# Performance work log

Measured on AMD Instinct MI355X. Metric: run time of the kernel, lower is better.

Reference implementation:

```python
import jax, jax.numpy as jnp
import numpy as np

# Module hyperparameters (init_kwargs)
THRESHOLD_ABS = 0.2
THRESHOLD_REL = 0.05   # set to None to disable the relative-threshold branch
MIN_DISTANCE = 3


def setup_inputs() -> dict:
    key = jax.random.key(0)
    # belief maps in [0, 1), NCHW
    belive_map = jax.random.uniform(key, (32, 4, 512, 512), dtype=jnp.float32)
    return {"belive_map": belive_map}


def reference(belive_map):
    """Peak detection on belief maps (dense, jit-friendly form).

    Faithful to BeliveMapsNMS.forward: the torch module additionally compacts
    the mask into (coords, labels, scores) lists via nonzero/gather, which has
    data-dependent shapes; here we return the equivalent dense outputs:
      mask        [B,C,H,W] bool   - peak locations (nonzero of this == torch ind)
      scores_abs  [B,C,H,W] f32    - belief value at peaks, 0 elsewhere
      scores_rel  [B,C,H,W] f32    - scores_abs / per-(b,c) max
    """
    k = 2 * MIN_DISTANCE + 1          # 7
    pad = k // 2                       # 3 -> 'same' max pool, stride 1

    # F.max_pool2d(kernel=k, stride=1, padding=k//2)
    x_max = jax.lax.reduce_window(
        belive_map, -jnp.inf, jax.lax.max,
        window_dimensions=(1, 1, k, k),
        window_strides=(1, 1, 1, 1),
        padding=[(0, 0), (0, 0), (pad, pad), (pad, pad)],
    )

    # per-(batch, channel) global max: hh.max(dim=2) on the flattened map
    vmax = jnp.max(belive_map, axis=(2, 3), keepdims=True)  # [B,C,1,1]

    mask = (x_max == belive_map) & (belive_map > THRESHOLD_ABS)
    if THRESHOLD_REL is not None:
        mask = mask & (belive_map > THRESHOLD_REL * vmax)

    scores_abs = jnp.where(mask, belive_map, jnp.float32(0.0))
    scores_rel = scores_abs / vmax
    return mask, scores_abs, scores_rel
```

## Files before the change

### kernel.cpp

```cpp
#include <hip/hip_runtime.h>
#include <math.h>


#define H 512
#define W 512
#define PLANE_ELEMS (H * W)
#define TH 16
#define NROWS 14
#define RW 520
#define NEG_INF (-INFINITY)
#define VCHUNKS 16

typedef float v4f __attribute__((ext_vector_type(4)));

__device__ __forceinline__ float4 vmax4(float4 a, float4 b) {
    return make_float4(fmaxf(a.x, b.x), fmaxf(a.y, b.y), fmaxf(a.z, b.z), fmaxf(a.w, b.w));
}

__device__ __forceinline__ void nt_store4(float* p, float a, float b, float c, float d) {
    v4f v = {a, b, c, d};
    __builtin_nontemporal_store(v, (v4f*)p);
}

__global__ __launch_bounds__(256) void vmax_kernel(const float* __restrict__ in,
                                                   float* __restrict__ partials) {
    const int chunk = blockIdx.x;
    const int plane = blockIdx.y;
    const float4* p = (const float4*)(in + (size_t)plane * PLANE_ELEMS) + chunk * 4096;
    float4 v[16];
    #pragma unroll
    for (int j = 0; j < 16; ++j) v[j] = p[threadIdx.x + (j << 8)];
    float4 t[8];
    #pragma unroll
    for (int j = 0; j < 8; ++j) t[j] = vmax4(v[j], v[j + 8]);
    #pragma unroll
    for (int j = 0; j < 4; ++j) t[j] = vmax4(t[j], t[j + 4]);
    float4 q = vmax4(vmax4(t[0], t[1]), vmax4(t[2], t[3]));
    float m = fmaxf(fmaxf(q.x, q.y), fmaxf(q.z, q.w));
    #pragma unroll
    for (int o = 32; o > 0; o >>= 1) m = fmaxf(m, __shfl_down(m, o, 64));
    __shared__ float s[4];
    if ((threadIdx.x & 63) == 0) s[threadIdx.x >> 6] = m;
    __syncthreads();
    if (threadIdx.x == 0) {
        partials[(plane << 4) + chunk] = fmaxf(fmaxf(s[0], s[1]), fmaxf(s[2], s[3]));
    }
}

__global__ __launch_bounds__(256, 4) void nms_kernel(const float* __restrict__ in,
                                                     const float* __restrict__ partials,
                                                     float* __restrict__ out, int N) {
    const int hwid = blockIdx.x + (blockIdx.y << 5);
    const int wg = ((hwid & 7) << 9) + (hwid >> 3);
    const int plane = wg >> 5;
    const int ty0 = (wg & 31) * TH;

    const float* pin = in + (size_t)plane * PLANE_ELEMS;

    __shared__ __align__(16) float sCol[TH * RW];

    const int cg = threadIdx.x & 127;
    const int strip = threadIdx.x >> 7;
    const int c = cg << 2;
    const int y0 = strip << 3;
    const int gy0 = ty0 + y0;

    float4 r[NROWS];
    #pragma unroll
    for (int k = 0; k < NROWS; ++k) {
        const int gy = gy0 + k - 3;
        if (gy >= 0 && gy < H) {
            r[k] = *(const float4*)(pin + (size_t)gy * W + c);
        } else {
            r[k] = make_float4(NEG_INF, NEG_INF, NEG_INF, NEG_INF);
        }
    }

    float4 A[7];
    A[6] = r[6];
    #pragma unroll
    for (int j = 5; j >= 0; --j) A[j] = vmax4(r[j], A[j + 1]);
    float4 cm[8];
    cm[0] = A[0];
    float4 Bv = r[7];
    cm[1] = vmax4(A[1], Bv);
    #pragma unroll
    for (int j = 2; j <= 6; ++j) { Bv = vmax4(Bv, r[j + 6]); cm[j] = vmax4(A[j], Bv); }
    Bv = vmax4(Bv, r[13]);
    cm[7] = Bv;

    #pragma unroll
    for (int i = 0; i < 8; ++i) {
        *(float4*)&sCol[(y0 + i) * RW + 4 + c] = cm[i];
    }
    if (threadIdx.x < TH) {
        *(float4*)&sCol[threadIdx.x * RW] =
            make_float4(NEG_INF, NEG_INF, NEG_INF, NEG_INF);
    } else if (threadIdx.x < 2 * TH) {
        *(float4*)&sCol[(threadIdx.x - TH) * RW + 4 + W] =
            make_float4(NEG_INF, NEG_INF, NEG_INF, NEG_INF);
    }

    float4 pm0 = *(const float4*)&partials[(plane << 4) + 0];
    float4 pm1 = *(const float4*)&partials[(plane << 4) + 4];
    float4 pm2 = *(const float4*)&partials[(plane << 4) + 8];
    float4 pm3 = *(const float4*)&partials[(plane << 4) + 12];
    float4 q = vmax4(vmax4(pm0, pm1), vmax4(pm2, pm3));
    const float vmax = fmaxf(fmaxf(q.x, q.y), fmaxf(q.z, q.w));
    const float rel_thr = 0.05f * vmax;
    const float inv_vmax = 1.0f / vmax;

    __syncthreads();

    float* __restrict__ omask = out;
    float* __restrict__ oabs = out + (size_t)N;
    float* __restrict__ orel = out + 2 * (size_t)N;

    #pragma unroll
    for (int i = 0; i < 8; ++i) {
        const int rowb = (y0 + i) * RW;
        const float4 lo = *(const float4*)&sCol[rowb + c];
        const float4 hi = *(const float4*)&sCol[rowb + c + 8];
        const float a0 = lo.y, a1 = lo.z, a2 = lo.w;
        const float a3 = cm[i].x, a4 = cm[i].y, a5 = cm[i].z, a6 = cm[i].w;
        const float a7 = hi.x, a8 = hi.y, a9 = hi.z;
        const float t5 = fmaxf(a5, a6), t4 = fmaxf(a4, t5), t3 = fmaxf(a3, t4);
        const float t2 = fmaxf(a2, t3), t1 = fmaxf(a1, t2), t0 = fmaxf(a0, t1);
        const float b2 = fmaxf(a7, a8), b3 = fmaxf(b2, a9);
        const float m0 = t0;
        const float m1 = fmaxf(t1, a7);
        const float m2 = fmaxf(t2, b2);
        const float m3 = fmaxf(t3, b3);

        const float4 cc = r[i + 3];
        const bool p0 = (m0 == cc.x) & (cc.x > 0.2f) & (cc.x > rel_thr);
        const bool p1 = (m1 == cc.y) & (cc.y > 0.2f) & (cc.y > rel_thr);
        const bool p2 = (m2 == cc.z) & (cc.z > 0.2f) & (cc.z > rel_thr);
        const bool p3 = (m3 == cc.w) & (cc.w > 0.2f) & (cc.w > rel_thr);
        const float a0s = p0 ? cc.x : 0.0f, a1s = p1 ? cc.y : 0.0f;
        const float a2s = p2 ? cc.z : 0.0f, a3s = p3 ? cc.w : 0.0f;
        const int gy = gy0 + i;
        const size_t o = (size_t)plane * PLANE_ELEMS + (size_t)gy * W + c;
        nt_store4(omask + o, p0 ? 1.0f : 0.0f, p1 ? 1.0f : 0.0f,
                             p2 ? 1.0f : 0.0f, p3 ? 1.0f : 0.0f);
        nt_store4(oabs + o, a0s, a1s, a2s, a3s);
        nt_store4(orel + o, a0s * inv_vmax, a1s * inv_vmax,
                            a2s * inv_vmax, a3s * inv_vmax);
    }
}

extern "C" void kernel_launch(void* const* d_in, const int* in_sizes, int n_in,
                              void* d_out, int out_size, void* d_ws, size_t ws_size,
                              hipStream_t stream) {
    const float* in = (const float*)d_in[0];
    float* out = (float*)d_out;
    const int N = in_sizes[0];
    const int planes = N / PLANE_ELEMS;

    float* partials = (float*)d_ws;

    vmax_kernel<<<dim3(VCHUNKS, planes), 256, 0, stream>>>(in, partials);
    nms_kernel<<<dim3(H / TH, planes), 256, 0, stream>>>(in, partials, out, N);
}
```

Baseline: 482.7 us.

## Replace LDS horizontal max with wavefront shuffles and 8-wide per-lane columns

The NMS kernel no longer stages vertical column maxima in shared memory with a block barrier. Each wavefront now owns a full 512-wide row band of 8 rows, and each lane holds 8 columns. Horizontal neighbours come from three shuffle-up and three shuffle-down exchanges per row. This removes the LDS traffic and __syncthreads but doubles register use per thread, so launch bounds drop to 2 blocks per SIMD and the grid becomes 16 blocks per plane. Edge rows are clamped and loaded unconditionally, then masked with -inf.

```diff
diff --git a/kernel.cpp b/kernel.cpp
--- a/kernel.cpp
+++ b/kernel.cpp
@@ -5,9 +5,6 @@
 #define H 512
 #define W 512
 #define PLANE_ELEMS (H * W)
-#define TH 16
-#define NROWS 14
-#define RW 520
 #define NEG_INF (-INFINITY)
 #define VCHUNKS 16
 
@@ -47,105 +44,112 @@
     }
 }
 
-__global__ __launch_bounds__(256, 4) void nms_kernel(const float* __restrict__ in,
+__global__ __launch_bounds__(256, 2) void nms_kernel(const float* __restrict__ in,
                                                      const float* __restrict__ partials,
                                                      float* __restrict__ out, int N) {
-    const int hwid = blockIdx.x + (blockIdx.y << 5);
-    const int wg = ((hwid & 7) << 9) + (hwid >> 3);
-    const int plane = wg >> 5;
-    const int ty0 = (wg & 31) * TH;
+    const int hwid = blockIdx.x + (blockIdx.y << 4);
+    const int wg = ((hwid & 7) << 8) + (hwid >> 3);
+    const int plane = wg >> 4;
+    const int wid = threadIdx.x >> 6;
+    const int lane = threadIdx.x & 63;
+    const int band = ((wg & 15) << 2) + wid;
+    const int gy0 = band << 3;
+    const int c = lane << 3;
 
     const float* pin = in + (size_t)plane * PLANE_ELEMS;
 
-    __shared__ __align__(16) float sCol[TH * RW];
-
-    const int cg = threadIdx.x & 127;
-    const int strip = threadIdx.x >> 7;
-    const int c = cg << 2;
-    const int y0 = strip << 3;
-    const int gy0 = ty0 + y0;
-
-    float4 r[NROWS];
+    float4 rA[14], rB[14];
     #pragma unroll
-    for (int k = 0; k < NROWS; ++k) {
+    for (int k = 0; k < 14; ++k) {
         const int gy = gy0 + k - 3;
-        if (gy >= 0 && gy < H) {
-            r[k] = *(const float4*)(pin + (size_t)gy * W + c);
-        } else {
-            r[k] = make_float4(NEG_INF, NEG_INF, NEG_INF, NEG_INF);
+        const int gyc = gy < 0 ? 0 : (gy > H - 1 ? H - 1 : gy);
+        const float* p = pin + (size_t)gyc * W + c;
+        float4 a = *(const float4*)p;
+        float4 b = *(const float4*)(p + 4);
+        if (gy != gyc) {
+            a = make_float4(NEG_INF, NEG_INF, NEG_INF, NEG_INF);
+            b = make_float4(NEG_INF, NEG_INF, NEG_INF, NEG_INF);
         }
+        rA[k] = a; rB[k] = b;
     }
 
-    float4 A[7];
-    A[6] = r[6];
-    #pragma unroll
-    for (int j = 5; j >= 0; --j) A[j] = vmax4(r[j], A[j + 1]);
-    float4 cm[8];
-    cm[0] = A[0];
-    float4 Bv = r[7];
-    cm[1] = vmax4(A[1], Bv);
-    #pragma unroll
-    for (int j = 2; j <= 6; ++j) { Bv = vmax4(Bv, r[j + 6]); cm[j] = vmax4(A[j], Bv); }
-    Bv = vmax4(Bv, r[13]);
-    cm[7] = Bv;
-
-    #pragma unroll
-    for (int i = 0; i < 8; ++i) {
-        *(float4*)&sCol[(y0 + i) * RW + 4 + c] = cm[i];
-    }
-    if (threadIdx.x < TH) {
-        *(float4*)&sCol[threadIdx.x * RW] =
-            make_float4(NEG_INF, NEG_INF, NEG_INF, NEG_INF);
-    } else if (threadIdx.x < 2 * TH) {
-        *(float4*)&sCol[(threadIdx.x - TH) * RW + 4 + W] =
-            make_float4(NEG_INF, NEG_INF, NEG_INF, NEG_INF);
-    }
-
-    float4 pm0 = *(const float4*)&partials[(plane << 4) + 0];
-    float4 pm1 = *(const float4*)&partials[(plane << 4) + 4];
-    float4 pm2 = *(const float4*)&partials[(plane << 4) + 8];
-    float4 pm3 = *(const float4*)&partials[(plane << 4) + 12];
-    float4 q = vmax4(vmax4(pm0, pm1), vmax4(pm2, pm3));
+    const float4 pm0 = *(const float4*)&partials[(plane << 4) + 0];
+    const float4 pm1 = *(const float4*)&partials[(plane << 4) + 4];
+    const float4 pm2 = *(const float4*)&partials[(plane << 4) + 8];
+    const float4 pm3 = *(const float4*)&partials[(plane << 4) + 12];
+    const float4 q = vmax4(vmax4(pm0, pm1), vmax4(pm2, pm3));
     const float vmax = fmaxf(fmaxf(q.x, q.y), fmaxf(q.z, q.w));
     const float rel_thr = 0.05f * vmax;
     const float inv_vmax = 1.0f / vmax;
 
-    __syncthreads();
+    float4 AA[7], AB[7];
+    AA[6] = rA[6]; AB[6] = rB[6];
+    #pragma unroll
+    for (int j = 5; j >= 0; --j) {
+        AA[j] = vmax4(rA[j], AA[j + 1]);
+        AB[j] = vmax4(rB[j], AB[j + 1]);
+    }
 
     float* __restrict__ omask = out;
     float* __restrict__ oabs = out + (size_t)N;
     float* __restrict__ orel = out + 2 * (size_t)N;
 
+    float4 BA, BB;
     #pragma unroll
     for (int i = 0; i < 8; ++i) {
-        const int rowb = (y0 + i) * RW;
-        const float4 lo = *(const float4*)&sCol[rowb + c];
-        const float4 hi = *(const float4*)&sCol[rowb + c + 8];
-        const float a0 = lo.y, a1 = lo.z, a2 = lo.w;
-        const float a3 = cm[i].x, a4 = cm[i].y, a5 = cm[i].z, a6 = cm[i].w;
-        const float a7 = hi.x, a8 = hi.y, a9 = hi.z;
-        const float t5 = fmaxf(a5, a6), t4 = fmaxf(a4, t5), t3 = fmaxf(a3, t4);
-        const float t2 = fmaxf(a2, t3), t1 = fmaxf(a1, t2), t0 = fmaxf(a0, t1);
-        const float b2 = fmaxf(a7, a8), b3 = fmaxf(b2, a9);
-        const float m0 = t0;
-        const float m1 = fmaxf(t1, a7);
-        const float m2 = fmaxf(t2, b2);
-        const float m3 = fmaxf(t3, b3);
+        float4 mA, mB;
+        if (i == 0) {
+            mA = AA[0]; mB = AB[0];
+        } else {
+            if (i == 1) { BA = rA[7]; BB = rB[7]; }
+            else        { BA = vmax4(BA, rA[i + 6]); BB = vmax4(BB, rB[i + 6]); }
+            if (i == 7) { mA = BA; mB = BB; }
+            else        { mA = vmax4(AA[i], BA); mB = vmax4(AB[i], BB); }
+        }
 
-        const float4 cc = r[i + 3];
-        const bool p0 = (m0 == cc.x) & (cc.x > 0.2f) & (cc.x > rel_thr);
-        const bool p1 = (m1 == cc.y) & (cc.y > 0.2f) & (cc.y > rel_thr);
-        const bool p2 = (m2 == cc.z) & (cc.z > 0.2f) & (cc.z > rel_thr);
-        const bool p3 = (m3 == cc.w) & (cc.w > 0.2f) & (cc.w > rel_thr);
-        const float a0s = p0 ? cc.x : 0.0f, a1s = p1 ? cc.y : 0.0f;
-        const float a2s = p2 ? cc.z : 0.0f, a3s = p3 ? cc.w : 0.0f;
+        float l0 = __shfl_up(mB.y, 1, 64), l1 = __shfl_up(mB.z, 1, 64), l2 = __shfl_up(mB.w, 1, 64);
+        float r0 = __shfl_down(mA.x, 1, 64), r1 = __shfl_down(mA.y, 1, 64), r2 = __shfl_down(mA.z, 1, 64);
+        if (lane == 0)  { l0 = NEG_INF; l1 = NEG_INF; l2 = NEG_INF; }
+        if (lane == 63) { r0 = NEG_INF; r1 = NEG_INF; r2 = NEG_INF; }
+        const float a[14] = {l0, l1, l2, mA.x, mA.y, mA.z, mA.w,
+                             mB.x, mB.y, mB.z, mB.w, r0, r1, r2};
+        float A[7];
+        A[6] = a[6];
+        #pragma unroll
+        for (int j = 5; j >= 0; --j) A[j] = fmaxf(a[j], A[j + 1]);
+        float hm[8];
+        hm[0] = A[0];
+        float Bh = a[7];
+        hm[1] = fmaxf(A[1], Bh);
+        #pragma unroll
+        for (int j = 2; j <= 6; ++j) { Bh = fmaxf(Bh, a[6 + j]); hm[j] = fmaxf(A[j], Bh); }
+        Bh = fmaxf(Bh, a[13]);
+        hm[7] = Bh;
+
+        const float4 cA = rA[i + 3], cB = rB[i + 3];
+        const bool p0 = (hm[0] == cA.x) & (cA.x > 0.2f) & (cA.x > rel_thr);
+        const bool p1 = (hm[1] == cA.y) & (cA.y > 0.2f) & (cA.y > rel_thr);
+        const bool p2 = (hm[2] == cA.z) & (cA.z > 0.2f) & (cA.z > rel_thr);
+        const bool p3 = (hm[3] == cA.w) & (cA.w > 0.2f) & (cA.w > rel_thr);
+        const bool p4 = (hm[4] == cB.x) & (cB.x > 0.2f) & (cB.x > rel_thr);
+        const bool p5 = (hm[5] == cB.y) & (cB.y > 0.2f) & (cB.y > rel_thr);
+        const bool p6 = (hm[6] == cB.z) & (cB.z > 0.2f) & (cB.z > rel_thr);
+        const bool p7 = (hm[7] == cB.w) & (cB.w > 0.2f) & (cB.w > rel_thr);
+        const float s0 = p0 ? cA.x : 0.0f, s1 = p1 ? cA.y : 0.0f;
+        const float s2 = p2 ? cA.z : 0.0f, s3 = p3 ? cA.w : 0.0f;
+        const float s4 = p4 ? cB.x : 0.0f, s5 = p5 ? cB.y : 0.0f;
+        const float s6 = p6 ? cB.z : 0.0f, s7 = p7 ? cB.w : 0.0f;
+
         const int gy = gy0 + i;
         const size_t o = (size_t)plane * PLANE_ELEMS + (size_t)gy * W + c;
-        nt_store4(omask + o, p0 ? 1.0f : 0.0f, p1 ? 1.0f : 0.0f,
-                             p2 ? 1.0f : 0.0f, p3 ? 1.0f : 0.0f);
-        nt_store4(oabs + o, a0s, a1s, a2s, a3s);
-        nt_store4(orel + o, a0s * inv_vmax, a1s * inv_vmax,
-                            a2s * inv_vmax, a3s * inv_vmax);
+        nt_store4(omask + o,     p0 ? 1.0f : 0.0f, p1 ? 1.0f : 0.0f,
+                                 p2 ? 1.0f : 0.0f, p3 ? 1.0f : 0.0f);
+        nt_store4(omask + o + 4, p4 ? 1.0f : 0.0f, p5 ? 1.0f : 0.0f,
+                                 p6 ? 1.0f : 0.0f, p7 ? 1.0f : 0.0f);
+        nt_store4(oabs + o,     s0, s1, s2, s3);
+        nt_store4(oabs + o + 4, s4, s5, s6, s7);
+        nt_store4(orel + o,     s0 * inv_vmax, s1 * inv_vmax, s2 * inv_vmax, s3 * inv_vmax);
+        nt_store4(orel + o + 4, s4 * inv_vmax, s5 * inv_vmax, s6 * inv_vmax, s7 * inv_vmax);
     }
 }
 
@@ -160,5 +164,5 @@
     float* partials = (float*)d_ws;
 
     vmax_kernel<<<dim3(VCHUNKS, planes), 256, 0, stream>>>(in, partials);
-    nms_kernel<<<dim3(H / TH, planes), 256, 0, stream>>>(in, partials, out, N);
+    nms_kernel<<<dim3(16, planes), 256, 0, stream>>>(in, partials, out, N);
 }
```

New measurement: 624.8 us. 1.29x slower.
